# Kernel optimization log

Measured on AMD Instinct MI355X. Metric: run time of the kernel, lower is better.

Reference implementation:

```python
import jax, jax.numpy as jnp
import numpy as np

EOS_IDX = 1
B, S, V, E, H = 32, 64, 32000, 512, 512


def _gru_step(x, h, w_ih, w_hh, b_ih, b_hh):
    # PyTorch GRU cell: gates ordered (r, z, n)
    gi = x @ w_ih.T + b_ih
    gh = h @ w_hh.T + b_hh
    i_r, i_z, i_n = jnp.split(gi, 3, axis=-1)
    h_r, h_z, h_n = jnp.split(gh, 3, axis=-1)
    r = jax.nn.sigmoid(i_r + h_r)
    z = jax.nn.sigmoid(i_z + h_z)
    n = jnp.tanh(i_n + r * h_n)
    return (1.0 - z) * n + z * h


def setup_inputs() -> dict:
    key = jax.random.key(0)
    ks = jax.random.split(key, 16)
    u = lambda k, shape: jax.random.uniform(k, shape, jnp.float32, -1.0, 1.0) / np.sqrt(H)
    return {
        "targets": jax.random.randint(ks[0], (B, S), 0, V),
        "targets_kws": jax.random.randint(ks[1], (B, S), 0, V),
        "sent_state": jax.random.normal(ks[2], (1, B, H), jnp.float32),
        "targets_len": jax.random.randint(ks[3], (B,), 1, S),
        "emb": jax.random.normal(ks[4], (V, E), jnp.float32) * 0.05,
        "w_ih_w": u(ks[5], (3 * H, 2 * E)),
        "w_hh_w": u(ks[6], (3 * H, H)),
        "b_ih_w": u(ks[7], (3 * H,)),
        "b_hh_w": u(ks[8], (3 * H,)),
        "w_ih_s": u(ks[9], (3 * H, H)),
        "w_hh_s": u(ks[10], (3 * H, H)),
        "b_ih_s": u(ks[11], (3 * H,)),
        "b_hh_s": u(ks[12], (3 * H,)),
        "out_w": u(ks[13], (V, H)),
        "out_b": u(ks[14], (V,)),
    }


def reference(targets, targets_kws, sent_state, targets_len,
              emb, w_ih_w, w_hh_w, b_ih_w, b_hh_w,
              w_ih_s, w_hh_s, b_ih_s, b_hh_s, out_w, out_b):
    seq = targets.shape[1]
    h0 = sent_state[0]  # nlayers = 1 -> (B, H)
    last_words = targets[:, :-1].T   # (S-1, B)
    keywords = targets_kws[:, 1:].T  # (S-1, B)
    next_words = targets[:, 1:].T    # (S-1, B)

    def step(carry, inp):
        word_h, sent_h = carry
        lw, kw, nw = inp
        x = jnp.concatenate([emb[kw], emb[lw]], axis=-1)  # (B, 2E)
        word_h = _gru_step(x, word_h, w_ih_w, w_hh_w, b_ih_w, b_hh_w)
        logp = jax.nn.log_softmax(word_h @ out_w.T + out_b, axis=-1)
        m = (nw == EOS_IDX).astype(word_h.dtype)[:, None]  # EOS mask
        tmp = _gru_step(word_h, sent_h, w_ih_s, w_hh_s, b_ih_s, b_hh_s)
        sent_h2 = sent_h * (1.0 - m) + tmp * m
        word_h2 = word_h * (1.0 - m) + tmp * m
        return (word_h2, sent_h2), logp

    _, logps = jax.lax.scan(step, (h0, h0), (last_words, keywords, next_words))
    # logps: (S-1, B, V). Masked NLL as in mask_loss().
    tok_logp = jnp.take_along_axis(logps, next_words[:, :, None], axis=2)[:, :, 0]
    valid = (targets_len[None, :] > jnp.arange(1, seq)[:, None]).astype(logps.dtype)
    return -(tok_logp * valid).sum()
```

## Files before the change

kernel.cpp:

```cpp
#include <hip/hip_runtime.h>
#include <stdint.h>

typedef short bf16x8 __attribute__((ext_vector_type(8)));
typedef float f32x4 __attribute__((ext_vector_type(4)));
typedef unsigned short u16;
typedef unsigned long long u64;

#define B_  32
#define S_  64
#define V_  32000
#define H_  512
#define T_  63
#define R_  2016
#define RP_ 2048
#define G3_ 1536
#define NWG 32
#define NWORK 192
#define NTILE 4000

#define o_X      0ull
#define o_Wih    4194304ull
#define o_OutW   7340032ull
#define o_PackHH 40108032ull
#define o_PackIS 41680896ull
#define o_PackHS 43253760ull
#define o_GI     44826624ull
#define o_WHf    57212928ull
#define o_WHb    61341696ull
#define o_HPUB   63438848ull
#define o_SPUB   63504384ull
#define o_ARR    63569920ull
#define o_CTR    63571968ull
#define o_PART   63733760ull
#define o_LSE    72122368ull
#define o_RL     72130560ull
#define o_FLG    72138752ull

__device__ __forceinline__ u16 f2b(float f) {
  unsigned u = __float_as_uint(f);
  u = (u + 0x7FFFu + ((u >> 16) & 1u)) >> 16;
  return (u16)u;
}
__device__ __forceinline__ float sigm(float x) { return 1.0f / (1.0f + __expf(-x)); }

__device__ __forceinline__ void fbar(int* arr, int ph, int tid) {
  __syncthreads();
  if (tid == 0) {
    __hip_atomic_fetch_add(&arr[ph], 1, __ATOMIC_RELAXED, __HIP_MEMORY_SCOPE_AGENT);
    while (__hip_atomic_load(&arr[ph], __ATOMIC_RELAXED, __HIP_MEMORY_SCOPE_AGENT) < NWG)
      __builtin_amdgcn_s_sleep(1);
  }
  __syncthreads();
}

__global__ __launch_bounds__(256) void k_cvt(const float* __restrict__ src,
                                             u16* __restrict__ dst, int n) {
  int i4 = (blockIdx.x * 256 + threadIdx.x) * 4;
  if (i4 < n) {
    float4 v = *(const float4*)(src + i4);
    u16 t[4] = {f2b(v.x), f2b(v.y), f2b(v.z), f2b(v.w)};
    *(uint2*)(dst + i4) = *(uint2*)t;
  }
}

__global__ __launch_bounds__(256) void k_pack(const float* __restrict__ w, u16* __restrict__ up) {
  int uid = blockIdx.x * 256 + threadIdx.x;
  int lane = uid & 63;
  int ksct = uid >> 6;
  int ks = ksct & 15, ct = ksct >> 4;
  int nrow = ct * 16 + (lane & 15);
  int k0 = ks * 32 + (lane >> 4) * 8;
  const float* p = w + (size_t)nrow * 512 + k0;
  float4 v0 = *(const float4*)p;
  float4 v1 = *(const float4*)(p + 4);
  u16 t[8] = {f2b(v0.x), f2b(v0.y), f2b(v0.z), f2b(v0.w),
              f2b(v1.x), f2b(v1.y), f2b(v1.z), f2b(v1.w)};
  *(uint4*)(up + (size_t)uid * 8) = *(uint4*)t;
}

__global__ __launch_bounds__(256) void k_gather(const float* __restrict__ emb,
                                                const int* __restrict__ tg,
                                                const int* __restrict__ tk,
                                                u16* __restrict__ X) {
  int r = blockIdx.x;
  int tid = threadIdx.x;
  u16* xr = X + (size_t)r * 1024;
  if (r < R_) {
    int t = r >> 5, b = r & 31;
    int kw = tk[b * 64 + t + 1];
    int lw = tg[b * 64 + t];
    const float* src = (tid < 128) ? (emb + (size_t)kw * 512 + tid * 4)
                                   : (emb + (size_t)lw * 512 + (tid - 128) * 4);
    float4 v = *(const float4*)src;
    u16 o[4] = {f2b(v.x), f2b(v.y), f2b(v.z), f2b(v.w)};
    *(uint2*)(xr + tid * 4) = *(uint2*)o;
  } else {
    u16 z[4] = {0, 0, 0, 0};
    *(uint2*)(xr + tid * 4) = *(uint2*)z;
  }
}

__global__ __launch_bounds__(256) void k_init(const float* __restrict__ sent,
                                              const int* __restrict__ tg,
                                              u64* __restrict__ hpub, u64* __restrict__ spub,
                                              u16* __restrict__ whb, int* __restrict__ flg,
                                              int* __restrict__ arr, int* __restrict__ ctr) {
  int idx = blockIdx.x * 256 + threadIdx.x;
  whb[(size_t)R_ * 512 + idx] = 0;
  if (idx < 2048) {
    int b = idx >> 6, c = idx & 63;
    const float* p = sent + (size_t)b * 512 + c * 8;
    float4 v0 = *(const float4*)p;
    float4 v1 = *(const float4*)(p + 4);
    u16 t[8] = {f2b(v0.x), f2b(v0.y), f2b(v0.z), f2b(v0.w),
                f2b(v1.x), f2b(v1.y), f2b(v1.z), f2b(v1.w)};
    int slot = c ^ (b & 7);
    u64* d = hpub + b * 128 + slot * 2;
    d[0] = ((const u64*)t)[0];
    d[1] = ((const u64*)t)[1];
    u64* s = spub + b * 128 + slot * 2;
    s[0] = ((const u64*)t)[0];
    s[1] = ((const u64*)t)[1];
  }
  if (blockIdx.x == 0 && threadIdx.x < 63) {
    int f = 0;
    for (int b = 0; b < 32; ++b) f |= (tg[b * 64 + threadIdx.x + 1] == 1);
    flg[threadIdx.x] = f;
  }
  if (blockIdx.x == 1) arr[threadIdx.x] = 0;
  if (blockIdx.x == 2) ctr[threadIdx.x] = 0;
}

__global__ __launch_bounds__(256) void k_gemm0(const u16* __restrict__ A, const u16* __restrict__ Bw,
                                               const float* __restrict__ bias, int N, int K, int nrt,
                                               float* __restrict__ outC, int Mstore) {
  __shared__ u16 As[128 * 64];
  __shared__ u16 Bs[128 * 64];
  int bid = blockIdx.x;
  int rt = bid % nrt, ct = bid / nrt;
  int m0 = rt * 128, n0 = ct * 128;
  int tid = threadIdx.x;
  int lane = tid & 63, wid = tid >> 6;
  int wr = wid >> 1, wc = wid & 1;
  f32x4 z = {0.f, 0.f, 0.f, 0.f};
  f32x4 acc[4][4];
#pragma unroll
  for (int i = 0; i < 4; ++i)
#pragma unroll
    for (int j = 0; j < 4; ++j) acc[i][j] = z;

  int nkt = K >> 6;
  for (int kt = 0; kt < nkt; ++kt) {
    __syncthreads();
#pragma unroll
    for (int it = 0; it < 4; ++it) {
      int idx = it * 256 + tid;
      int row = idx >> 3;
      int kch = idx & 7;
      int sch = kch ^ (row & 7);
      *(uint4*)(&As[row * 64 + kch * 8]) =
          *(const uint4*)(A + (size_t)(m0 + row) * K + kt * 64 + sch * 8);
      *(uint4*)(&Bs[row * 64 + kch * 8]) =
          *(const uint4*)(Bw + (size_t)(n0 + row) * K + kt * 64 + sch * 8);
    }
    __syncthreads();
#pragma unroll
    for (int kk = 0; kk < 2; ++kk) {
      bf16x8 af[4], bf[4];
#pragma unroll
      for (int i = 0; i < 4; ++i) {
        int row = wr * 64 + i * 16 + (lane & 15);
        int c = kk * 4 + (lane >> 4);
        af[i] = *(const bf16x8*)(&As[row * 64 + ((c ^ (row & 7)) * 8)]);
      }
#pragma unroll
      for (int j = 0; j < 4; ++j) {
        int row = wc * 64 + j * 16 + (lane & 15);
        int c = kk * 4 + (lane >> 4);
        bf[j] = *(const bf16x8*)(&Bs[row * 64 + ((c ^ (row & 7)) * 8)]);
      }
#pragma unroll
      for (int i = 0; i < 4; ++i)
#pragma unroll
        for (int j = 0; j < 4; ++j)
          acc[i][j] = __builtin_amdgcn_mfma_f32_16x16x32_bf16(af[i], bf[j], acc[i][j], 0, 0, 0);
    }
  }
#pragma unroll
  for (int i = 0; i < 4; ++i) {
    int mb = m0 + wr * 64 + i * 16 + ((lane >> 4) << 2);
#pragma unroll
    for (int j = 0; j < 4; ++j) {
      int n = n0 + wc * 64 + j * 16 + (lane & 15);
      float bb = bias[n];
#pragma unroll
      for (int r = 0; r < 4; ++r) {
        int m = mb + r;
        if (m < Mstore) outC[(size_t)m * N + n] = acc[i][j][r] + bb;
      }
    }
  }
}

struct RecurSM {
  u16 hb[32 * 512];
  u16 wls[3 * 1024 * 8];
  float ghl[6][32][16];
  float gil[2][3][32][16];
  float hloc[32][16];
  float sloc[32][16];
  u16 hps[32][16];
  u16 sps[32][16];
};
struct GemmSM {
  u16 As[128 * 64];
  u16 Bs[128 * 64];
};
union MegaSM {
  RecurSM r;
  GemmSM g;
};

__device__ __forceinline__ f32x4 mm16_lds(const u16* hb, const u16* bl, int lane, int rt) {
  f32x4 a0 = {0.f, 0.f, 0.f, 0.f}, a1 = {0.f, 0.f, 0.f, 0.f};
  int row = rt * 16 + (lane & 15);
  int cb = lane >> 4;
#pragma unroll
  for (int ks = 0; ks < 16; ks += 2) {
    int c0 = ks * 4 + cb, c1 = c0 + 4;
    bf16x8 av0 = *(const bf16x8*)(&hb[row * 512 + ((c0 ^ (row & 7)) * 8)]);
    bf16x8 bv0 = *(const bf16x8*)(&bl[(ks * 64 + lane) * 8]);
    bf16x8 av1 = *(const bf16x8*)(&hb[row * 512 + ((c1 ^ (row & 7)) * 8)]);
    bf16x8 bv1 = *(const bf16x8*)(&bl[((ks + 1) * 64 + lane) * 8]);
    a0 = __builtin_amdgcn_mfma_f32_16x16x32_bf16(av0, bv0, a0, 0, 0, 0);
    a1 = __builtin_amdgcn_mfma_f32_16x16x32_bf16(av1, bv1, a1, 0, 0, 0);
  }
  return a0 + a1;
}

__device__ __forceinline__ f32x4 mm16g(const u16* hb, const u16* bp, int lane, int rt) {
  f32x4 acc = {0.f, 0.f, 0.f, 0.f};
#pragma unroll
  for (int ks = 0; ks < 16; ++ks) {
    int row = rt * 16 + (lane & 15);
    int c = ks * 4 + (lane >> 4);
    bf16x8 a = *(const bf16x8*)(&hb[row * 512 + ((c ^ (row & 7)) * 8)]);
    bf16x8 b = *(const bf16x8*)(bp + (size_t)(ks * 64 + lane) * 8);
    acc = __builtin_amdgcn_mfma_f32_16x16x32_bf16(a, b, acc, 0, 0, 0);
  }
  return acc;
}

__device__ __forceinline__ void gemm_tile(u16* As, u16* Bs, const u16* __restrict__ A,
                                          const u16* __restrict__ Bw,
                                          const float* __restrict__ bias,
                                          int rt, int ct, float2* __restrict__ parts, int tid) {
  int m0 = rt * 128, n0 = ct * 128;
  int lane = tid & 63, wid = tid >> 6;
  int wr = wid >> 1, wc = wid & 1;
  f32x4 z = {0.f, 0.f, 0.f, 0.f};
  f32x4 acc[2][4];
#pragma unroll
  for (int i = 0; i < 2; ++i)
#pragma unroll
    for (int j = 0; j < 4; ++j) acc[i][j] = z;

  for (int kt = 0; kt < 8; ++kt) {
    __syncthreads();
#pragma unroll
    for (int it = 0; it < 2; ++it) {
      int idx = it * 512 + tid;
      int row = idx >> 3, kch = idx & 7;
      *(uint4*)(&As[row * 64 + kch * 8]) =
          *(const uint4*)(A + (size_t)(m0 + row) * 512 + kt * 64 + kch * 8);
      int sch = kch ^ (row & 7);
      *(uint4*)(&Bs[row * 64 + kch * 8]) =
          *(const uint4*)(Bw + (size_t)(n0 + row) * 512 + kt * 64 + sch * 8);
    }
    __syncthreads();
#pragma unroll
    for (int kk = 0; kk < 2; ++kk) {
      bf16x8 af[2], bf[4];
#pragma unroll
      for (int i = 0; i < 2; ++i) {
        int row = wr * 32 + i * 16 + (lane & 15);
        int c = kk * 4 + (lane >> 4);
        af[i] = *(const bf16x8*)(&As[row * 64 + ((c ^ (row & 7)) * 8)]);
      }
#pragma unroll
      for (int j = 0; j < 4; ++j) {
        int row = wc * 64 + j * 16 + (lane & 15);
        int c = kk * 4 + (lane >> 4);
        bf[j] = *(const bf16x8*)(&Bs[row * 64 + ((c ^ (row & 7)) * 8)]);
      }
#pragma unroll
      for (int i = 0; i < 2; ++i)
#pragma unroll
        for (int j = 0; j < 4; ++j)
          acc[i][j] = __builtin_amdgcn_mfma_f32_16x16x32_bf16(af[i], bf[j], acc[i][j], 0, 0, 0);
    }
  }
  float bb[4];
#pragma unroll
  for (int j = 0; j < 4; ++j) bb[j] = bias[n0 + wc * 64 + j * 16 + (lane & 15)];
  int chunk = ct * 2 + wc;
#pragma unroll
  for (int i = 0; i < 2; ++i) {
#pragma unroll
    for (int r = 0; r < 4; ++r) {
      float l0 = acc[i][0][r] + bb[0], l1 = acc[i][1][r] + bb[1];
      float l2 = acc[i][2][r] + bb[2], l3 = acc[i][3][r] + bb[3];
      float mx = fmaxf(fmaxf(l0, l1), fmaxf(l2, l3));
#pragma unroll
      for (int d = 1; d < 16; d <<= 1) mx = fmaxf(mx, __shfl_xor(mx, d));
      float s = __expf(l0 - mx) + __expf(l1 - mx) + __expf(l2 - mx) + __expf(l3 - mx);
#pragma unroll
      for (int d = 1; d < 16; d <<= 1) s += __shfl_xor(s, d);
      if ((lane & 15) == 0) {
        int m = m0 + wr * 32 + i * 16 + ((lane >> 4) << 2) + r;
        parts[(size_t)m * 512 + chunk] = make_float2(mx, s);
      }
    }
  }
}

__global__ __launch_bounds__(512) void k_mega(
    const float* __restrict__ gi, const u16* __restrict__ packHH, const u16* __restrict__ packIS,
    const u16* __restrict__ packHS, const float* __restrict__ bhh_w, const float* __restrict__ bih_s,
    const float* __restrict__ bhh_s, const int* __restrict__ targets, const int* __restrict__ flags,
    const float* __restrict__ sent, u64* __restrict__ hpub, u64* __restrict__ spub,
    float* __restrict__ whf, u16* __restrict__ whb, int* __restrict__ arr, int* __restrict__ ctr,
    const u16* __restrict__ outw16, const float* __restrict__ outb, float2* __restrict__ parts) {
  __shared__ MegaSM sm;
  const int tid = threadIdx.x;
  int* steps = ctr + 32;

  if (blockIdx.x >= NWG) {
    const int w = blockIdx.x - NWG;
    for (int k = 0;; ++k) {
      int tile = w + k * NWORK;
      if (tile >= NTILE) break;
      int rt = tile / 250;
      int ct = tile - rt * 250;
      if (tid == 0) {
        int need = 4 * rt + 4;
        if (need > T_) need = T_;
        while (__hip_atomic_load(steps, __ATOMIC_ACQUIRE, __HIP_MEMORY_SCOPE_AGENT) < need)
          __builtin_amdgcn_s_sleep(64);
      }
      gemm_tile(sm.g.As, sm.g.Bs, whb, outw16, outb, rt, ct, parts, tid);
      __syncthreads();
    }
    return;
  }

  const int lane = tid & 63;
  const int wid = tid >> 6;
  const int gate = wid >> 1;
  const int rt = wid & 1;
  const int g = blockIdx.x;
  const int b_ = tid >> 4, hl = tid & 15;
  const int n_ = g * 16 + hl;

  {
    const uint4* src = (const uint4*)packHH;
    uint4* dst = (uint4*)sm.r.wls;
    for (int lin = tid; lin < 3072; lin += 512) {
      int which = lin >> 10, off = lin & 1023;
      dst[lin] = src[(size_t)(which * 32 + g) * 1024 + off];
    }
  }
  {
    float v = sent[(size_t)b_ * 512 + n_];
    sm.r.hloc[b_][hl] = v;
    sm.r.sloc[b_][hl] = v;
  }
  if (wid >= 6) {
    int lid = tid - 384;
    const float* base = gi + (size_t)g * 16;
#pragma unroll
    for (int q = 0; q < 3; ++q) {
      int fid = q * 128 + lid;
      int ga = fid >> 7, rem = fid & 127;
      int b = rem >> 2, h4 = (rem & 3) << 2;
      *(float4*)&sm.r.gil[0][ga][b][h4] = *(const float4*)(base + (size_t)b * 1536 + ga * 512 + h4);
    }
  }
  const float bw_r = bhh_w[n_], bw_z = bhh_w[512 + n_], bw_n = bhh_w[1024 + n_];
  __syncthreads();

  int ph = 0;
  int scur = 0;
  for (int t = 0; t < T_; ++t) {
    const int cur = t & 1, nxt = cur ^ 1;
    {
      const u64* src = hpub + cur * 4096;
      u64* d = (u64*)sm.r.hb;
      for (int idx = tid; idx < 4096; idx += 512)
        d[idx] = __hip_atomic_load(&src[idx], __ATOMIC_RELAXED, __HIP_MEMORY_SCOPE_AGENT);
    }
    __syncthreads();
    if (wid < 6) {
      f32x4 acc = mm16_lds(sm.r.hb, sm.r.wls + gate * 8192, lane, rt);
      int bb = rt * 16 + ((lane >> 4) << 2);
      int cl = lane & 15;
#pragma unroll
      for (int r4 = 0; r4 < 4; ++r4) sm.r.ghl[gate][bb + r4][cl] = acc[r4];
    } else if (t + 1 < T_) {
      int lid = tid - 384;
      const float* base = gi + (size_t)(t + 1) * 32 * 1536 + g * 16;
#pragma unroll
      for (int q = 0; q < 3; ++q) {
        int fid = q * 128 + lid;
        int ga = fid >> 7, rem = fid & 127;
        int b = rem >> 2, h4 = (rem & 3) << 2;
        *(float4*)&sm.r.gil[nxt][ga][b][h4] =
            *(const float4*)(base + (size_t)b * 1536 + ga * 512 + h4);
      }
    }
    __syncthreads();
    {
      int rrow = t * 32 + b_;
      float r_ = sigm(sm.r.gil[cur][0][b_][hl] + sm.r.ghl[0][b_][hl] + bw_r);
      float z_ = sigm(sm.r.gil[cur][1][b_][hl] + sm.r.ghl[1][b_][hl] + bw_z);
      float nn = tanhf(sm.r.gil[cur][2][b_][hl] + r_ * (sm.r.ghl[2][b_][hl] + bw_n));
      float hold = sm.r.hloc[b_][hl];
      float hnew = (1.f - z_) * nn + z_ * hold;
      sm.r.hloc[b_][hl] = hnew;
      sm.r.hps[b_][hl] = f2b(hnew);
      whf[(size_t)rrow * 512 + n_] = hnew;
    }
    __syncthreads();
    if (tid < 128) {
      int b = tid >> 2, j = tid & 3, q = j >> 1, half = j & 1;
      u64 v = *(const u64*)&sm.r.hps[b][q * 8 + half * 4];
      int slot = (2 * g + q) ^ (b & 7);
      __hip_atomic_store(&hpub[nxt * 4096 + b * 128 + slot * 2 + half], v,
                         __ATOMIC_RELAXED, __HIP_MEMORY_SCOPE_AGENT);
    } else if (tid < 256) {
      int l = tid - 128;
      int b = l >> 2, j = l & 3, q = j >> 1, half = j & 1;
      u64 v = *(const u64*)&sm.r.hps[b][q * 8 + half * 4];
      int slot = (2 * g + q) ^ (b & 7);
      __hip_atomic_store((u64*)whb + (size_t)(t * 32 + b) * 128 + slot * 2 + half, v,
                         __ATOMIC_RELAXED, __HIP_MEMORY_SCOPE_AGENT);
    }
    fbar(arr, ph, tid); ++ph;
    if (g == 0 && tid == 0)
      __hip_atomic_store(steps, t + 1, __ATOMIC_RELEASE, __HIP_MEMORY_SCOPE_AGENT);

    if (flags[t]) {
      {
        const u64* src = hpub + nxt * 4096;
        u64* d = (u64*)sm.r.hb;
        for (int idx = tid; idx < 4096; idx += 512)
          d[idx] = __hip_atomic_load(&src[idx], __ATOMIC_RELAXED, __HIP_MEMORY_SCOPE_AGENT);
      }
      fbar(arr, ph, tid); ++ph;
      f32x4 ax = {0.f, 0.f, 0.f, 0.f};
      if (wid < 6) ax = mm16g(sm.r.hb, packIS + (size_t)(gate * 32 + g) * 8192, lane, rt);
      __syncthreads();
      {
        const u64* src = spub + scur * 4096;
        u64* d = (u64*)sm.r.hb;
        for (int idx = tid; idx < 4096; idx += 512)
          d[idx] = __hip_atomic_load(&src[idx], __ATOMIC_RELAXED, __HIP_MEMORY_SCOPE_AGENT);
      }
      __syncthreads();
      if (wid < 6) {
        f32x4 ah = mm16g(sm.r.hb, packHS + (size_t)(gate * 32 + g) * 8192, lane, rt);
        int bb = rt * 16 + ((lane >> 4) << 2);
        int cl = lane & 15;
#pragma unroll
        for (int r4 = 0; r4 < 4; ++r4) {
          sm.r.ghl[gate][bb + r4][cl] = ax[r4];
          sm.r.ghl[3 + gate][bb + r4][cl] = ah[r4];
        }
      }
      __syncthreads();
      {
        float r_ = sigm(sm.r.ghl[0][b_][hl] + bih_s[n_] + sm.r.ghl[3][b_][hl] + bhh_s[n_]);
        float z_ = sigm(sm.r.ghl[1][b_][hl] + bih_s[512 + n_] + sm.r.ghl[4][b_][hl] + bhh_s[512 + n_]);
        float nn = tanhf(sm.r.ghl[2][b_][hl] + bih_s[1024 + n_] +
                         r_ * (sm.r.ghl[5][b_][hl] + bhh_s[1024 + n_]));
        float hs = sm.r.sloc[b_][hl];
        float tmpv = (1.f - z_) * nn + z_ * hs;
        int m = (targets[b_ * 64 + t + 1] == 1);
        float hw = sm.r.hloc[b_][hl];
        float hw2 = m ? tmpv : hw;
        float hs2 = m ? tmpv : hs;
        sm.r.hloc[b_][hl] = hw2;
        sm.r.sloc[b_][hl] = hs2;
        sm.r.hps[b_][hl] = f2b(hw2);
        sm.r.sps[b_][hl] = f2b(hs2);
      }
      __syncthreads();
      if (tid < 128) {
        int b = tid >> 2, j = tid & 3, q = j >> 1, half = j & 1;
        int slot = (2 * g + q) ^ (b & 7);
        u64 v = *(const u64*)&sm.r.hps[b][q * 8 + half * 4];
        __hip_atomic_store(&hpub[nxt * 4096 + b * 128 + slot * 2 + half], v,
                           __ATOMIC_RELAXED, __HIP_MEMORY_SCOPE_AGENT);
        u64 w2 = *(const u64*)&sm.r.sps[b][q * 8 + half * 4];
        __hip_atomic_store(&spub[(scur ^ 1) * 4096 + b * 128 + slot * 2 + half], w2,
                           __ATOMIC_RELAXED, __HIP_MEMORY_SCOPE_AGENT);
      }
      scur ^= 1;
      fbar(arr, ph, tid); ++ph;
    }
  }
}

__global__ __launch_bounds__(256) void k_lse(const float2* __restrict__ parts,
                                             float* __restrict__ lse) {
  int wid = threadIdx.x >> 6, lane = threadIdx.x & 63;
  int row = blockIdx.x * 4 + wid;
  if (row >= R_) return;
  float m = -3.0e38f, s = 0.f;
  for (int c = lane; c < 500; c += 64) {
    float2 p = parts[(size_t)row * 512 + c];
    float nm = fmaxf(m, p.x);
    s = s * __expf(m - nm) + p.y * __expf(p.x - nm);
    m = nm;
  }
#pragma unroll
  for (int d = 1; d < 64; d <<= 1) {
    float om = __shfl_xor(m, d), os = __shfl_xor(s, d);
    float nm = fmaxf(m, om);
    s = s * __expf(m - nm) + os * __expf(om - nm);
    m = nm;
  }
  if (lane == 0) lse[row] = m + __logf(s);
}

__global__ __launch_bounds__(256) void k_rowloss(const float* __restrict__ whf,
                                                 const float* __restrict__ outw,
                                                 const float* __restrict__ outb,
                                                 const int* __restrict__ targets,
                                                 const int* __restrict__ tlen,
                                                 const float* __restrict__ lse,
                                                 float* __restrict__ rl) {
  int wid = threadIdx.x >> 6, lane = threadIdx.x & 63;
  int r = blockIdx.x * 4 + wid;
  if (r >= R_) return;
  int t = r >> 5, b = r & 31;
  int nw = targets[b * 64 + t + 1];
  const float* hv = whf + (size_t)r * 512;
  const float* wv = outw + (size_t)nw * 512;
  float acc = 0.f;
#pragma unroll
  for (int q = 0; q < 2; ++q) {
    int k = lane * 8 + q * 4;
    float4 a = *(const float4*)(hv + k);
    float4 w = *(const float4*)(wv + k);
    acc += a.x * w.x + a.y * w.y + a.z * w.z + a.w * w.w;
  }
#pragma unroll
  for (int d = 1; d < 64; d <<= 1) acc += __shfl_xor(acc, d);
  if (lane == 0) {
    bool valid = tlen[b] > (t + 1);
    rl[r] = valid ? (lse[r] - (acc + outb[nw])) : 0.f;
  }
}

__global__ __launch_bounds__(256) void k_sum(const float* __restrict__ rl, float* __restrict__ out) {
  __shared__ float sm[256];
  float a = 0.f;
  for (int i = threadIdx.x; i < R_; i += 256) a += rl[i];
  sm[threadIdx.x] = a;
  __syncthreads();
  for (int s = 128; s > 0; s >>= 1) {
    if (threadIdx.x < s) sm[threadIdx.x] += sm[threadIdx.x + s];
    __syncthreads();
  }
  if (threadIdx.x == 0) out[0] = sm[0];
}

extern "C" void kernel_launch(void* const* d_in, const int* in_sizes, int n_in,
                              void* d_out, int out_size, void* d_ws, size_t ws_size,
                              hipStream_t stream) {
  const int* targets = (const int*)d_in[0];
  const int* tkws    = (const int*)d_in[1];
  const float* sent  = (const float*)d_in[2];
  const int* tlen    = (const int*)d_in[3];
  const float* emb   = (const float*)d_in[4];
  const float* wihw  = (const float*)d_in[5];
  const float* whhw  = (const float*)d_in[6];
  const float* bihw  = (const float*)d_in[7];
  const float* bhhw  = (const float*)d_in[8];
  const float* wihs  = (const float*)d_in[9];
  const float* whhs  = (const float*)d_in[10];
  const float* bihs  = (const float*)d_in[11];
  const float* bhhs  = (const float*)d_in[12];
  const float* outw  = (const float*)d_in[13];
  const float* outb  = (const float*)d_in[14];
  float* out = (float*)d_out;
  char* ws = (char*)d_ws;

  u16* X       = (u16*)(ws + o_X);
  u16* Wih16   = (u16*)(ws + o_Wih);
  u16* OutW16  = (u16*)(ws + o_OutW);
  u16* PackHH  = (u16*)(ws + o_PackHH);
  u16* PackIS  = (u16*)(ws + o_PackIS);
  u16* PackHS  = (u16*)(ws + o_PackHS);
  float* GI    = (float*)(ws + o_GI);
  float* WHf   = (float*)(ws + o_WHf);
  u16* WHb     = (u16*)(ws + o_WHb);
  u64* HPUB    = (u64*)(ws + o_HPUB);
  u64* SPUB    = (u64*)(ws + o_SPUB);
  int* ARR     = (int*)(ws + o_ARR);
  int* CTR     = (int*)(ws + o_CTR);
  float2* PART = (float2*)(ws + o_PART);
  float* LSE   = (float*)(ws + o_LSE);
  float* RL    = (float*)(ws + o_RL);
  int* FLG     = (int*)(ws + o_FLG);

  k_cvt<<<dim3(16000), dim3(256), 0, stream>>>(outw, OutW16, V_ * H_);
  k_cvt<<<dim3(1536), dim3(256), 0, stream>>>(wihw, Wih16, G3_ * 1024);
  k_pack<<<dim3(384), dim3(256), 0, stream>>>(whhw, PackHH);
  k_pack<<<dim3(384), dim3(256), 0, stream>>>(wihs, PackIS);
  k_pack<<<dim3(384), dim3(256), 0, stream>>>(whhs, PackHS);
  k_gather<<<dim3(RP_), dim3(256), 0, stream>>>(emb, targets, tkws, X);
  k_init<<<dim3(64), dim3(256), 0, stream>>>(sent, targets, HPUB, SPUB, WHb, FLG, ARR, CTR);

  k_gemm0<<<dim3(16 * 12), dim3(256), 0, stream>>>(X, Wih16, bihw, G3_, 1024, 16, GI, R_);

  k_mega<<<dim3(NWG + NWORK), dim3(512), 0, stream>>>(GI, PackHH, PackIS, PackHS, bhhw, bihs, bhhs,
                                                      targets, FLG, sent, HPUB, SPUB, WHf, WHb,
                                                      ARR, CTR, OutW16, outb, PART);

  k_lse<<<dim3(504), dim3(256), 0, stream>>>(PART, LSE);
  k_rowloss<<<dim3(504), dim3(256), 0, stream>>>(WHf, outw, outb, targets, tlen, LSE, RL);
  k_sum<<<dim3(1), dim3(256), 0, stream>>>(RL, out);
}
```

Before: 413.3 us.

## Fold input-gate GEMM and output-weight conversion into the persistent mega kernel

Removes the separate k_gemm0 launch and the full output-weight bf16 conversion launch. The 192 worker blocks of k_mega now compute the input-gate GEMM tiles and publish per-row-tile completion counters, and the recurrence blocks wait on those counters before reading GI. Each worker also converts its own output-weight column tiles to bf16 while the recurrence runs, then processes its fixed column tiles per row tile instead of striding over a global tile list. This overlaps preprocessing with the serial recurrence and cuts launch gaps, at the cost of extra spin-waits on agent-scope atomics and a static assignment of output tiles to workers.

```diff
diff --git a/kernel.cpp b/kernel.cpp
--- a/kernel.cpp
+++ b/kernel.cpp
@@ -16,7 +16,6 @@
 #define G3_ 1536
 #define NWG 32
 #define NWORK 192
-#define NTILE 4000
 
 #define o_X      0ull
 #define o_Wih    4194304ull
@@ -131,77 +130,6 @@
   if (blockIdx.x == 2) ctr[threadIdx.x] = 0;
 }
 
-__global__ __launch_bounds__(256) void k_gemm0(const u16* __restrict__ A, const u16* __restrict__ Bw,
-                                               const float* __restrict__ bias, int N, int K, int nrt,
-                                               float* __restrict__ outC, int Mstore) {
-  __shared__ u16 As[128 * 64];
-  __shared__ u16 Bs[128 * 64];
-  int bid = blockIdx.x;
-  int rt = bid % nrt, ct = bid / nrt;
-  int m0 = rt * 128, n0 = ct * 128;
-  int tid = threadIdx.x;
-  int lane = tid & 63, wid = tid >> 6;
-  int wr = wid >> 1, wc = wid & 1;
-  f32x4 z = {0.f, 0.f, 0.f, 0.f};
-  f32x4 acc[4][4];
-#pragma unroll
-  for (int i = 0; i < 4; ++i)
-#pragma unroll
-    for (int j = 0; j < 4; ++j) acc[i][j] = z;
-
-  int nkt = K >> 6;
-  for (int kt = 0; kt < nkt; ++kt) {
-    __syncthreads();
-#pragma unroll
-    for (int it = 0; it < 4; ++it) {
-      int idx = it * 256 + tid;
-      int row = idx >> 3;
-      int kch = idx & 7;
-      int sch = kch ^ (row & 7);
-      *(uint4*)(&As[row * 64 + kch * 8]) =
-          *(const uint4*)(A + (size_t)(m0 + row) * K + kt * 64 + sch * 8);
-      *(uint4*)(&Bs[row * 64 + kch * 8]) =
-          *(const uint4*)(Bw + (size_t)(n0 + row) * K + kt * 64 + sch * 8);
-    }
-    __syncthreads();
-#pragma unroll
-    for (int kk = 0; kk < 2; ++kk) {
-      bf16x8 af[4], bf[4];
-#pragma unroll
-      for (int i = 0; i < 4; ++i) {
-        int row = wr * 64 + i * 16 + (lane & 15);
-        int c = kk * 4 + (lane >> 4);
-        af[i] = *(const bf16x8*)(&As[row * 64 + ((c ^ (row & 7)) * 8)]);
-      }
-#pragma unroll
-      for (int j = 0; j < 4; ++j) {
-        int row = wc * 64 + j * 16 + (lane & 15);
-        int c = kk * 4 + (lane >> 4);
-        bf[j] = *(const bf16x8*)(&Bs[row * 64 + ((c ^ (row & 7)) * 8)]);
-      }
-#pragma unroll
-      for (int i = 0; i < 4; ++i)
-#pragma unroll
-        for (int j = 0; j < 4; ++j)
-          acc[i][j] = __builtin_amdgcn_mfma_f32_16x16x32_bf16(af[i], bf[j], acc[i][j], 0, 0, 0);
-    }
-  }
-#pragma unroll
-  for (int i = 0; i < 4; ++i) {
-    int mb = m0 + wr * 64 + i * 16 + ((lane >> 4) << 2);
-#pragma unroll
-    for (int j = 0; j < 4; ++j) {
-      int n = n0 + wc * 64 + j * 16 + (lane & 15);
-      float bb = bias[n];
-#pragma unroll
-      for (int r = 0; r < 4; ++r) {
-        int m = mb + r;
-        if (m < Mstore) outC[(size_t)m * N + n] = acc[i][j][r] + bb;
-      }
-    }
-  }
-}
-
 struct RecurSM {
   u16 hb[32 * 512];
   u16 wls[3 * 1024 * 8];
@@ -251,13 +179,80 @@
   return acc;
 }
 
+__device__ __forceinline__ void gi_tile(u16* As, u16* Bs, const u16* __restrict__ A,
+                                        const u16* __restrict__ Bw, const float* __restrict__ bias,
+                                        int rtm, int ctn, float* __restrict__ outC, int tid) {
+  int m0 = rtm * 128, n0 = ctn * 128;
+  int lane = tid & 63, wid = tid >> 6;
+  int wr = wid >> 1, wc = wid & 1;
+  f32x4 z = {0.f, 0.f, 0.f, 0.f};
+  f32x4 acc[2][4];
+#pragma unroll
+  for (int i = 0; i < 2; ++i)
+#pragma unroll
+    for (int j = 0; j < 4; ++j) acc[i][j] = z;
+
+  for (int kt = 0; kt < 16; ++kt) {
+    __syncthreads();
+#pragma unroll
+    for (int it = 0; it < 2; ++it) {
+      int idx = it * 512 + tid;
+      int row = idx >> 3, kch = idx & 7;
+      int sch = kch ^ (row & 7);
+      *(uint4*)(&As[row * 64 + kch * 8]) =
+          *(const uint4*)(A + (size_t)(m0 + row) * 1024 + kt * 64 + sch * 8);
+      *(uint4*)(&Bs[row * 64 + kch * 8]) =
+          *(const uint4*)(Bw + (size_t)(n0 + row) * 1024 + kt * 64 + sch * 8);
+    }
+    __syncthreads();
+#pragma unroll
+    for (int kk = 0; kk < 2; ++kk) {
+      bf16x8 af[2], bf[4];
+#pragma unroll
+      for (int i = 0; i < 2; ++i) {
+        int row = wr * 32 + i * 16 + (lane & 15);
+        int c = kk * 4 + (lane >> 4);
+        af[i] = *(const bf16x8*)(&As[row * 64 + ((c ^ (row & 7)) * 8)]);
+      }
+#pragma unroll
+      for (int j = 0; j < 4; ++j) {
+        int row = wc * 64 + j * 16 + (lane & 15);
+        int c = kk * 4 + (lane >> 4);
+        bf[j] = *(const bf16x8*)(&Bs[row * 64 + ((c ^ (row & 7)) * 8)]);
+      }
+#pragma unroll
+      for (int i = 0; i < 2; ++i)
+#pragma unroll
+        for (int j = 0; j < 4; ++j)
+          acc[i][j] = __builtin_amdgcn_mfma_f32_16x16x32_bf16(af[i], bf[j], acc[i][j], 0, 0, 0);
+    }
+  }
+#pragma unroll
+  for (int i = 0; i < 2; ++i) {
+    int mb = m0 + wr * 32 + i * 16 + ((lane >> 4) << 2);
+#pragma unroll
+    for (int j = 0; j < 4; ++j) {
+      int n = n0 + wc * 64 + j * 16 + (lane & 15);
+      float bb = bias[n];
+#pragma unroll
+      for (int r = 0; r < 4; ++r) {
+        int m = mb + r;
+        if (m < R_)
+          __hip_atomic_store(&outC[(size_t)m * 1536 + n], acc[i][j][r] + bb,
+                             __ATOMIC_RELAXED, __HIP_MEMORY_SCOPE_AGENT);
+      }
+    }
+  }
+}
+
 __device__ __forceinline__ void gemm_tile(u16* As, u16* Bs, const u16* __restrict__ A,
                                           const u16* __restrict__ Bw,
                                           const float* __restrict__ bias,
                                           int rt, int ct, float2* __restrict__ parts, int tid) {
   int m0 = rt * 128, n0 = ct * 128;
   int lane = tid & 63, wid = tid >> 6;
-  int wr = wid >> 1, wc = wid & 1;
+  int wr = wid >> 2, wc = wid & 3;
+  wr = wid >> 1; wc = wid & 1;
   f32x4 z = {0.f, 0.f, 0.f, 0.f};
   f32x4 acc[2][4];
 #pragma unroll
@@ -325,30 +320,52 @@
 }
 
 __global__ __launch_bounds__(512) void k_mega(
-    const float* __restrict__ gi, const u16* __restrict__ packHH, const u16* __restrict__ packIS,
+    float* __restrict__ gi, const u16* __restrict__ packHH, const u16* __restrict__ packIS,
     const u16* __restrict__ packHS, const float* __restrict__ bhh_w, const float* __restrict__ bih_s,
     const float* __restrict__ bhh_s, const int* __restrict__ targets, const int* __restrict__ flags,
     const float* __restrict__ sent, u64* __restrict__ hpub, u64* __restrict__ spub,
     float* __restrict__ whf, u16* __restrict__ whb, int* __restrict__ arr, int* __restrict__ ctr,
-    const u16* __restrict__ outw16, const float* __restrict__ outb, float2* __restrict__ parts) {
+    u16* __restrict__ outw16, const float* __restrict__ outw, const float* __restrict__ outb,
+    const u16* __restrict__ X, const u16* __restrict__ wih16, const float* __restrict__ bihw,
+    float2* __restrict__ parts) {
   __shared__ MegaSM sm;
   const int tid = threadIdx.x;
   int* steps = ctr + 32;
+  int* rowdone = ctr + 64;
 
   if (blockIdx.x >= NWG) {
     const int w = blockIdx.x - NWG;
-    for (int k = 0;; ++k) {
-      int tile = w + k * NWORK;
-      if (tile >= NTILE) break;
-      int rt = tile / 250;
-      int ct = tile - rt * 250;
+    {
+      int rtm = w & 15, ctn = w >> 4;
+      gi_tile(sm.g.As, sm.g.Bs, X, wih16, bihw, rtm, ctn, gi, tid);
+      __syncthreads();
+      if (tid == 0)
+        __hip_atomic_fetch_add(&rowdone[rtm], 1, __ATOMIC_RELEASE, __HIP_MEMORY_SCOPE_AGENT);
+    }
+    const int nown = (w < 58) ? 2 : 1;
+#pragma unroll
+    for (int p = 0; p < 2; ++p) {
+      if (p < nown) {
+        int ct = w + p * 192;
+        const float* src = outw + (size_t)ct * 65536;
+        u16* dst = outw16 + (size_t)ct * 65536;
+        for (int it = 0; it < 32; ++it) {
+          int e = it * 512 + tid;
+          float4 v = *(const float4*)(src + (size_t)e * 4);
+          u16 t[4] = {f2b(v.x), f2b(v.y), f2b(v.z), f2b(v.w)};
+          *(uint2*)(dst + (size_t)e * 4) = *(uint2*)t;
+        }
+      }
+    }
+    for (int rt = 0; rt < 16; ++rt) {
       if (tid == 0) {
         int need = 4 * rt + 4;
         if (need > T_) need = T_;
         while (__hip_atomic_load(steps, __ATOMIC_ACQUIRE, __HIP_MEMORY_SCOPE_AGENT) < need)
-          __builtin_amdgcn_s_sleep(64);
-      }
-      gemm_tile(sm.g.As, sm.g.Bs, whb, outw16, outb, rt, ct, parts, tid);
+          __builtin_amdgcn_s_sleep(32);
+      }
+      for (int p = 0; p < nown; ++p)
+        gemm_tile(sm.g.As, sm.g.Bs, whb, outw16, outb, rt, w + p * 192, parts, tid);
       __syncthreads();
     }
     return;
@@ -375,6 +392,11 @@
     sm.r.hloc[b_][hl] = v;
     sm.r.sloc[b_][hl] = v;
   }
+  if (tid == 0) {
+    while (__hip_atomic_load(&rowdone[0], __ATOMIC_ACQUIRE, __HIP_MEMORY_SCOPE_AGENT) < 12)
+      __builtin_amdgcn_s_sleep(8);
+  }
+  __syncthreads();
   if (wid >= 6) {
     int lid = tid - 384;
     const float* base = gi + (size_t)g * 16;
@@ -393,6 +415,11 @@
   int scur = 0;
   for (int t = 0; t < T_; ++t) {
     const int cur = t & 1, nxt = cur ^ 1;
+    if (tid == 0 && t + 1 < T_ && ((t + 1) & 3) == 0) {
+      int row = (t + 1) >> 2;
+      while (__hip_atomic_load(&rowdone[row], __ATOMIC_ACQUIRE, __HIP_MEMORY_SCOPE_AGENT) < 12)
+        __builtin_amdgcn_s_sleep(8);
+    }
     {
       const u64* src = hpub + cur * 4096;
       u64* d = (u64*)sm.r.hb;
@@ -615,7 +642,6 @@
   float* RL    = (float*)(ws + o_RL);
   int* FLG     = (int*)(ws + o_FLG);
 
-  k_cvt<<<dim3(16000), dim3(256), 0, stream>>>(outw, OutW16, V_ * H_);
   k_cvt<<<dim3(1536), dim3(256), 0, stream>>>(wihw, Wih16, G3_ * 1024);
   k_pack<<<dim3(384), dim3(256), 0, stream>>>(whhw, PackHH);
   k_pack<<<dim3(384), dim3(256), 0, stream>>>(wihs, PackIS);
@@ -623,11 +649,10 @@
   k_gather<<<dim3(RP_), dim3(256), 0, stream>>>(emb, targets, tkws, X);
   k_init<<<dim3(64), dim3(256), 0, stream>>>(sent, targets, HPUB, SPUB, WHb, FLG, ARR, CTR);
 
-  k_gemm0<<<dim3(16 * 12), dim3(256), 0, stream>>>(X, Wih16, bihw, G3_, 1024, 16, GI, R_);
-
   k_mega<<<dim3(NWG + NWORK), dim3(512), 0, stream>>>(GI, PackHH, PackIS, PackHS, bhhw, bihs, bhhs,
                                                       targets, FLG, sent, HPUB, SPUB, WHf, WHb,
-                                                      ARR, CTR, OutW16, outb, PART);
+                                                      ARR, CTR, OutW16, outw, outb,
+                                                      X, Wih16, bihw, PART);
 
   k_lse<<<dim3(504), dim3(256), 0, stream>>>(PART, LSE);
   k_rowloss<<<dim3(504), dim3(256), 0, stream>>>(WHf, outw, outb, targets, tlen, LSE, RL);
```

After: 565.0 us. 1.37x slower.

## Replace per-step grid barrier with per-workgroup progress flags

Applied to the files above, without the earlier changes.

The end-of-step atomic counter barrier across the 32 recurrent workgroups is replaced by per-workgroup monotonic step flags, each padded to its own cache line. At the start of the next step one wavefront polls all 32 flags until every workgroup has reached the current step. For non-EOS steps this removes one full barrier and the separate step-counter publish. The signal to the GEMM workers is now derived from the flag wait. Relaxed stores after __syncthreads carry the risk of weaker memory ordering for the hpub data, and the double-buffer hazard now relies on flag ordering.

```diff
diff --git a/kernel.cpp b/kernel.cpp
--- a/kernel.cpp
+++ b/kernel.cpp
@@ -35,6 +35,7 @@
 #define o_LSE    72122368ull
 #define o_RL     72130560ull
 #define o_FLG    72138752ull
+#define o_HFLG   72139776ull
 
 __device__ __forceinline__ u16 f2b(float f) {
   unsigned u = __float_as_uint(f);
@@ -104,7 +105,8 @@
                                               const int* __restrict__ tg,
                                               u64* __restrict__ hpub, u64* __restrict__ spub,
                                               u16* __restrict__ whb, int* __restrict__ flg,
-                                              int* __restrict__ arr, int* __restrict__ ctr) {
+                                              int* __restrict__ arr, int* __restrict__ ctr,
+                                              int* __restrict__ hflg) {
   int idx = blockIdx.x * 256 + threadIdx.x;
   whb[(size_t)R_ * 512 + idx] = 0;
   if (idx < 2048) {
@@ -129,6 +131,8 @@
   }
   if (blockIdx.x == 1) arr[threadIdx.x] = 0;
   if (blockIdx.x == 2) ctr[threadIdx.x] = 0;
+  if (blockIdx.x == 3) hflg[threadIdx.x] = 0;
+  if (blockIdx.x == 4) hflg[256 + threadIdx.x] = 0;
 }
 
 __global__ __launch_bounds__(256) void k_gemm0(const u16* __restrict__ A, const u16* __restrict__ Bw,
@@ -330,7 +334,8 @@
     const float* __restrict__ bhh_s, const int* __restrict__ targets, const int* __restrict__ flags,
     const float* __restrict__ sent, u64* __restrict__ hpub, u64* __restrict__ spub,
     float* __restrict__ whf, u16* __restrict__ whb, int* __restrict__ arr, int* __restrict__ ctr,
-    const u16* __restrict__ outw16, const float* __restrict__ outb, float2* __restrict__ parts) {
+    int* __restrict__ hflg, const u16* __restrict__ outw16, const float* __restrict__ outb,
+    float2* __restrict__ parts) {
   __shared__ MegaSM sm;
   const int tid = threadIdx.x;
   int* steps = ctr + 32;
@@ -393,6 +398,18 @@
   int scur = 0;
   for (int t = 0; t < T_; ++t) {
     const int cur = t & 1, nxt = cur ^ 1;
+    if (wid == 0) {
+      for (;;) {
+        int f = (lane < 32)
+            ? __hip_atomic_load(&hflg[lane * 16], __ATOMIC_RELAXED, __HIP_MEMORY_SCOPE_AGENT)
+            : 0x7fffffff;
+        if (__all(f >= t)) break;
+        __builtin_amdgcn_s_sleep(1);
+      }
+      if (g == 0 && lane == 0)
+        __hip_atomic_store(steps, t, __ATOMIC_RELEASE, __HIP_MEMORY_SCOPE_AGENT);
+    }
+    __syncthreads();
     {
       const u64* src = hpub + cur * 4096;
       u64* d = (u64*)sm.r.hb;
@@ -445,11 +462,13 @@
       __hip_atomic_store((u64*)whb + (size_t)(t * 32 + b) * 128 + slot * 2 + half, v,
                          __ATOMIC_RELAXED, __HIP_MEMORY_SCOPE_AGENT);
     }
-    fbar(arr, ph, tid); ++ph;
-    if (g == 0 && tid == 0)
-      __hip_atomic_store(steps, t + 1, __ATOMIC_RELEASE, __HIP_MEMORY_SCOPE_AGENT);
-
-    if (flags[t]) {
+
+    if (!flags[t]) {
+      __syncthreads();
+      if (tid == 0)
+        __hip_atomic_store(&hflg[g * 16], t + 1, __ATOMIC_RELAXED, __HIP_MEMORY_SCOPE_AGENT);
+    } else {
+      fbar(arr, ph, tid); ++ph;
       {
         const u64* src = hpub + nxt * 4096;
         u64* d = (u64*)sm.r.hb;
@@ -506,8 +525,21 @@
                            __ATOMIC_RELAXED, __HIP_MEMORY_SCOPE_AGENT);
       }
       scur ^= 1;
-      fbar(arr, ph, tid); ++ph;
-    }
+      __syncthreads();
+      if (tid == 0)
+        __hip_atomic_store(&hflg[g * 16], t + 1, __ATOMIC_RELAXED, __HIP_MEMORY_SCOPE_AGENT);
+    }
+  }
+  if (g == 0 && wid == 0) {
+    for (;;) {
+      int f = (lane < 32)
+          ? __hip_atomic_load(&hflg[lane * 16], __ATOMIC_RELAXED, __HIP_MEMORY_SCOPE_AGENT)
+          : 0x7fffffff;
+      if (__all(f >= T_)) break;
+      __builtin_amdgcn_s_sleep(1);
+    }
+    if (lane == 0)
+      __hip_atomic_store(steps, T_, __ATOMIC_RELEASE, __HIP_MEMORY_SCOPE_AGENT);
   }
 }
 
@@ -614,6 +646,7 @@
   float* LSE   = (float*)(ws + o_LSE);
   float* RL    = (float*)(ws + o_RL);
   int* FLG     = (int*)(ws + o_FLG);
+  int* HFLG    = (int*)(ws + o_HFLG);
 
   k_cvt<<<dim3(16000), dim3(256), 0, stream>>>(outw, OutW16, V_ * H_);
   k_cvt<<<dim3(1536), dim3(256), 0, stream>>>(wihw, Wih16, G3_ * 1024);
@@ -621,13 +654,13 @@
   k_pack<<<dim3(384), dim3(256), 0, stream>>>(wihs, PackIS);
   k_pack<<<dim3(384), dim3(256), 0, stream>>>(whhs, PackHS);
   k_gather<<<dim3(RP_), dim3(256), 0, stream>>>(emb, targets, tkws, X);
-  k_init<<<dim3(64), dim3(256), 0, stream>>>(sent, targets, HPUB, SPUB, WHb, FLG, ARR, CTR);
+  k_init<<<dim3(64), dim3(256), 0, stream>>>(sent, targets, HPUB, SPUB, WHb, FLG, ARR, CTR, HFLG);
 
   k_gemm0<<<dim3(16 * 12), dim3(256), 0, stream>>>(X, Wih16, bihw, G3_, 1024, 16, GI, R_);
 
   k_mega<<<dim3(NWG + NWORK), dim3(512), 0, stream>>>(GI, PackHH, PackIS, PackHS, bhhw, bihs, bhhs,
                                                       targets, FLG, sent, HPUB, SPUB, WHf, WHb,
-                                                      ARR, CTR, OutW16, outb, PART);
+                                                      ARR, CTR, HFLG, OutW16, outb, PART);
 
   k_lse<<<dim3(504), dim3(256), 0, stream>>>(PART, LSE);
   k_rowloss<<<dim3(504), dim3(256), 0, stream>>>(WHf, outw, outb, targets, tlen, LSE, RL);
```

New measurement: 423.9 us. 1.03x slower.
